# Optimization experiments

Measured on AMD Instinct MI355X. Metric: run time of the kernel, lower is better.

## Reference

```python
import jax, jax.numpy as jnp
import numpy as np

DIM = 768
NUM_HEADS = 12
DIM_HEAD = 64
INNER = NUM_HEADS * DIM_HEAD  # 768
SCALE = DIM_HEAD ** -0.5


def setup_inputs() -> dict:
    key = jax.random.key(0)
    k1, k2, k3 = jax.random.split(key, 3)
    B, N = 8, 1024
    x = jax.random.normal(k1, (B, N, DIM), dtype=jnp.float32)
    # Linear(dim, 3*inner_dim, bias=False): weight shape (out, in) torch-style
    w_qkv = jax.random.normal(k2, (3 * INNER, DIM), dtype=jnp.float32) * (DIM ** -0.5)
    # proj: Linear(inner_dim, dim, bias=False)
    w_proj = jax.random.normal(k3, (DIM, INNER), dtype=jnp.float32) * (INNER ** -0.5)
    return {"x": x, "w_qkv": w_qkv, "w_proj": w_proj}


def reference(x, w_qkv, w_proj):
    B, N, C = x.shape
    H, dh = NUM_HEADS, DIM_HEAD
    # qkv projection: (B,N,C) @ (C, 3*inner) -> (B,N,3*inner)
    qkv = jnp.einsum('bnc,oc->bno', x, w_qkv)
    qkv = qkv.reshape(B, N, 3, H, dh).transpose(2, 0, 3, 1, 4)  # (3,B,H,N,dh)
    q, k, v = qkv[0], qkv[1], qkv[2]
    # attention scores (B,H,N,N)
    attn_scores = jnp.einsum('bhnd,bhmd->bhnm', q, k) * SCALE
    attn_probs = jax.nn.softmax(attn_scores, axis=-1)
    # attention output (B,H,N,dh) -> (B,N,inner)
    attn_out = jnp.einsum('bhnm,bhmd->bhnd', attn_probs, v)
    attn_out = attn_out.transpose(0, 2, 1, 3).reshape(B, N, H * dh)
    out = jnp.einsum('bni,oi->bno', attn_out, w_proj)
    return out
```

## Files before the change

kernel.cpp:

```cpp
#include <hip/hip_runtime.h>
#include <stdint.h>

typedef unsigned short u16;
typedef __attribute__((ext_vector_type(8))) short short8;
typedef __attribute__((ext_vector_type(4))) float f32x4;

#define LOG2E 1.44269504088896340736f

#define Bb 8
#define NSEQ 1024
#define DIMC 768
#define NH 12
#define DH 64
#define INNER 768
#define MTOT (Bb*NSEQ)
#define QKVN (3*INNER)
#define HEADS_TOT (Bb*NH)
#define QKV_PART ((size_t)Bb*NH*NSEQ*DH)

static __device__ inline u16 f2bf(float f) {
    uint32_t u = __builtin_bit_cast(uint32_t, f);
    uint32_t r = (u + 0x7fffu + ((u >> 16) & 1u)) >> 16;
    return (u16)r;
}

typedef __attribute__((address_space(1))) const void gas_void;
typedef __attribute__((address_space(3))) void las_void;
static __device__ __forceinline__ void async16(u16* lds, const u16* g) {
    __builtin_amdgcn_global_load_lds((gas_void*)(uintptr_t)g,
                                     (las_void*)(uintptr_t)lds, 16, 0, 0);
}

#define NX8  786432
#define NWQ8 221184
#define NWP8 73728
#define NCVT (NX8 + NWQ8 + NWP8)
__global__ __launch_bounds__(256) void cvt_all(const float* __restrict__ x,
                                               const float* __restrict__ wq,
                                               const float* __restrict__ wp,
                                               u16* __restrict__ xb,
                                               u16* __restrict__ wqb,
                                               u16* __restrict__ wpb) {
    int i = blockIdx.x * 256 + threadIdx.x;
    const float* s; u16* d; int j;
    if (i < NX8) { s = x; d = xb; j = i; }
    else if (i < NX8 + NWQ8) { s = wq; d = wqb; j = i - NX8; }
    else { s = wp; d = wpb; j = i - NX8 - NWQ8; }
    const float4* s4 = (const float4*)s;
    float4 a = s4[2 * j], b = s4[2 * j + 1];
    float v[8] = {a.x, a.y, a.z, a.w, b.x, b.y, b.z, b.w};
    u16 o[8];
#pragma unroll
    for (int t = 0; t < 8; t++) o[t] = f2bf(v[t]);
    ((uint4*)d)[j] = *(const uint4*)o;
}

#define BM 128
#define BN 128
#define BK 32

template <int MODE>
__global__ __launch_bounds__(256) void gemm_bt(const u16* __restrict__ A,
                                               const u16* __restrict__ Bm,
                                               void* __restrict__ Cout,
                                               int M, int N, int K) {
    __shared__ u16 As[BM * BK];
    __shared__ u16 Bs[BN * BK];
    const int tid = threadIdx.x;
    const int w = tid >> 6, lane = tid & 63, quad = lane >> 4, l16 = lane & 15;
    const int wr = w >> 1, wc = w & 1;
    const int m0 = blockIdx.y * BM;
    const int n0 = blockIdx.x * BN;

    const int rl = lane >> 2, cc = lane & 3;
    const u16* ag[2]; const u16* bg[2]; u16* al[2]; u16* bl[2];
#pragma unroll
    for (int j = 0; j < 2; j++) {
        int r = w * 32 + j * 16 + rl;
        int c = ((cc - ((r >> 1) & 3)) & 3) * 8;
        ag[j] = A + (size_t)(m0 + r) * K + c;
        bg[j] = Bm + (size_t)(n0 + r) * K + c;
        al[j] = As + (w * 32 + j * 16) * BK;
        bl[j] = Bs + (w * 32 + j * 16) * BK;
    }

    const int swz = ((quad + ((l16 >> 1) & 3)) & 3) * 8;
    int aoff[4], boff[4];
#pragma unroll
    for (int t = 0; t < 4; t++) {
        aoff[t] = (wr * 64 + t * 16 + l16) * BK + swz;
        boff[t] = (wc * 64 + t * 16 + l16) * BK + swz;
    }

    f32x4 acc[4][4] = {};
    for (int kt = 0; kt < K; kt += BK) {
        __syncthreads();
#pragma unroll
        for (int j = 0; j < 2; j++) {
            async16(al[j], ag[j] + kt);
            async16(bl[j], bg[j] + kt);
        }
        __syncthreads();
        short8 af[4], bf[4];
#pragma unroll
        for (int t = 0; t < 4; t++) af[t] = *(const short8*)(As + aoff[t]);
#pragma unroll
        for (int t = 0; t < 4; t++) bf[t] = *(const short8*)(Bs + boff[t]);
#pragma unroll
        for (int mt = 0; mt < 4; mt++)
#pragma unroll
            for (int nt = 0; nt < 4; nt++)
                acc[mt][nt] = __builtin_amdgcn_mfma_f32_16x16x32_bf16(af[mt], bf[nt],
                                                                      acc[mt][nt], 0, 0, 0);
    }

    if (MODE == 0) {
        u16* qkv = (u16*)Cout;
#pragma unroll
        for (int nt = 0; nt < 4; nt++) {
            int o = n0 + wc * 64 + nt * 16 + l16;
            int which = o / 768;
            int rem = o - which * 768;
            int h = rem >> 6, d = rem & 63;
            if (which == 2) {
                u16* vt = qkv + 2 * QKV_PART;
#pragma unroll
                for (int mt = 0; mt < 4; mt++) {
                    int m = m0 + wr * 64 + mt * 16 + quad * 4;
                    int bb = m >> 10, ns = m & 1023;
                    alignas(8) u16 pk[4];
#pragma unroll
                    for (int r = 0; r < 4; r++) pk[r] = f2bf(acc[mt][nt][r]);
                    *(uint2*)(vt + ((size_t)(bb * NH + h) * DH + d) * NSEQ + ns) =
                        *(const uint2*)pk;
                }
            } else {
                float sc = (which == 0) ? (0.125f * LOG2E) : 1.0f;
#pragma unroll
                for (int mt = 0; mt < 4; mt++)
#pragma unroll
                    for (int r = 0; r < 4; r++) {
                        int m = m0 + wr * 64 + mt * 16 + quad * 4 + r;
                        int bb = m >> 10, ns = m & 1023;
                        size_t idx = (size_t)which * QKV_PART +
                                     (((size_t)(bb * NH + h) * NSEQ + ns) << 6) + d;
                        qkv[idx] = f2bf(acc[mt][nt][r] * sc);
                    }
            }
        }
    } else {
        float* Co = (float*)Cout;
#pragma unroll
        for (int mt = 0; mt < 4; mt++)
#pragma unroll
            for (int nt = 0; nt < 4; nt++) {
                int o = n0 + wc * 64 + nt * 16 + l16;
#pragma unroll
                for (int r = 0; r < 4; r++) {
                    int m = m0 + wr * 64 + mt * 16 + quad * 4 + r;
                    Co[(size_t)m * N + o] = acc[mt][nt][r];
                }
            }
    }
}

__global__ __launch_bounds__(256) void attn_kernel(const u16* __restrict__ qkv,
                                                   u16* __restrict__ attn) {
    __shared__ u16 Ks[64 * 64];
    __shared__ u16 Vs[64 * 64];
    __shared__ u16 Plds[4][32 * 72];

    const int tid = threadIdx.x;
    const int w = tid >> 6, lane = tid & 63, quad = lane >> 4, l16 = lane & 15;
    const int bh = blockIdx.y;
    const int qt = blockIdx.x;
    const size_t headoff = (size_t)bh * NSEQ * DH;
    const u16* Qp = qkv + headoff;
    const u16* Kp = qkv + QKV_PART + headoff;
    const u16* Vtp = qkv + 2 * QKV_PART + headoff;
    const int q0 = qt * 128 + w * 32;

    const int rl8 = lane >> 3, cc8 = lane & 7;
    const u16* kg[2]; const u16* vg[2]; u16* kl[2]; u16* vl[2];
#pragma unroll
    for (int j = 0; j < 2; j++) {
        int r = w * 16 + j * 8 + rl8;
        int c = ((cc8 - r) & 7) * 8;
        kg[j] = Kp + (size_t)r * DH + c;
        vg[j] = Vtp + (size_t)r * NSEQ + c;
        kl[j] = Ks + (w * 16 + j * 8) * 64;
        vl[j] = Vs + (w * 16 + j * 8) * 64;
    }

    const int sw0 = ((quad + l16) & 7) * 8;
    const int sw1 = ((quad + 4 + l16) & 7) * 8;

    short8 qf[2][2];
#pragma unroll
    for (int mf = 0; mf < 2; mf++) {
        qf[mf][0] = *(const short8*)(Qp + (size_t)(q0 + mf * 16 + l16) * DH + quad * 8);
        qf[mf][1] = *(const short8*)(Qp + (size_t)(q0 + mf * 16 + l16) * DH + 32 + quad * 8);
    }

    f32x4 oacc[2][4] = {};
    float lsum[2][4] = {};

    for (int kt = 0; kt < NSEQ; kt += 64) {
        __syncthreads();
#pragma unroll
        for (int j = 0; j < 2; j++) {
            async16(kl[j], kg[j] + (size_t)kt * DH);
            async16(vl[j], vg[j] + kt);
        }
        __syncthreads();

        u16* Pw0 = Plds[w];
#pragma unroll
        for (int mf = 0; mf < 2; mf++) {
            f32x4 s[4];
#pragma unroll
            for (int nt = 0; nt < 4; nt++) {
                const u16* kr = Ks + (nt * 16 + l16) * 64;
                short8 kf0 = *(const short8*)(kr + sw0);
                short8 kf1 = *(const short8*)(kr + sw1);
                f32x4 z = {};
                z = __builtin_amdgcn_mfma_f32_16x16x32_bf16(qf[mf][0], kf0, z, 0, 0, 0);
                z = __builtin_amdgcn_mfma_f32_16x16x32_bf16(qf[mf][1], kf1, z, 0, 0, 0);
                s[nt] = z;
            }

            u16* Pw = Pw0 + mf * 16 * 72;
#pragma unroll
            for (int nt = 0; nt < 4; nt++)
#pragma unroll
                for (int r = 0; r < 4; r++) {
                    float p = __builtin_amdgcn_exp2f(s[nt][r]);
                    lsum[mf][r] += p;
                    Pw[(quad * 4 + r) * 72 + nt * 16 + l16] = f2bf(p);
                }
            short8 pa0 = *(const short8*)(Pw + l16 * 72 + quad * 8);
            short8 pa1 = *(const short8*)(Pw + l16 * 72 + 32 + quad * 8);

#pragma unroll
            for (int nt = 0; nt < 4; nt++) {
                const u16* vr = Vs + (nt * 16 + l16) * 64;
                short8 vf0 = *(const short8*)(vr + sw0);
                short8 vf1 = *(const short8*)(vr + sw1);
                oacc[mf][nt] = __builtin_amdgcn_mfma_f32_16x16x32_bf16(pa0, vf0,
                                                                       oacc[mf][nt], 0, 0, 0);
                oacc[mf][nt] = __builtin_amdgcn_mfma_f32_16x16x32_bf16(pa1, vf1,
                                                                       oacc[mf][nt], 0, 0, 0);
            }
        }
    }

#pragma unroll
    for (int mf = 0; mf < 2; mf++)
#pragma unroll
        for (int r = 0; r < 4; r++) {
            float v = lsum[mf][r];
#pragma unroll
            for (int mask = 1; mask < 16; mask <<= 1)
                v += __shfl_xor(v, mask, 16);
            lsum[mf][r] = 1.0f / v;
        }

    const int b = bh / NH, h = bh - (bh / NH) * NH;
#pragma unroll
    for (int mf = 0; mf < 2; mf++)
#pragma unroll
        for (int nt = 0; nt < 4; nt++)
#pragma unroll
            for (int r = 0; r < 4; r++) {
                int q = q0 + mf * 16 + quad * 4 + r;
                int d = nt * 16 + l16;
                float val = oacc[mf][nt][r] * lsum[mf][r];
                attn[((size_t)(b * NSEQ + q)) * INNER + h * DH + d] = f2bf(val);
            }
}

extern "C" void kernel_launch(void* const* d_in, const int* in_sizes, int n_in,
                              void* d_out, int out_size, void* d_ws, size_t ws_size,
                              hipStream_t stream) {
    const float* x = (const float*)d_in[0];
    const float* w_qkv = (const float*)d_in[1];
    const float* w_proj = (const float*)d_in[2];
    float* out = (float*)d_out;

    u16* xb = (u16*)d_ws;
    u16* wqkvb = xb + 6291456;
    u16* wprojb = wqkvb + 1769472;
    u16* qkvb = wprojb + 589824;
    u16* attnb = qkvb + 18874368;

    cvt_all<<<NCVT / 256, 256, 0, stream>>>(x, w_qkv, w_proj, xb, wqkvb, wprojb);

    dim3 g1(QKVN / BN, MTOT / BM);
    gemm_bt<0><<<g1, 256, 0, stream>>>(xb, wqkvb, qkvb, MTOT, QKVN, DIMC);

    dim3 g2(NSEQ / 128, HEADS_TOT);
    attn_kernel<<<g2, 256, 0, stream>>>(qkvb, attnb);

    dim3 g3(INNER / BN, MTOT / BM);
    gemm_bt<1><<<g3, 256, 0, stream>>>(attnb, wprojb, out, MTOT, INNER, DIMC);
}
```

Baseline: 205.9 us.

## Keep attention probabilities in registers via transposed S and widen QKV GEMM tile

The attention kernel now computes S transposed (K as the A operand, Q as B), so each lane's exp2 outputs line up with the 16x16x16 bf16 MFMA operand layout. P then feeds the PV product straight from registers, which removes the per-wave LDS round trip for P. K and V fragments are loaded once per key tile and shared across both query sub-tiles. The QKV GEMM moves to a 128x256 tile with 512 threads, and the output conversion uses packed bf16 stores. The costs are higher register pressure and a bf16 rounding change (round-half-up through pkbf), plus a fallback inline-asm MFMA path if the builtin is missing.

```diff
diff --git a/kernel.cpp b/kernel.cpp
--- a/kernel.cpp
+++ b/kernel.cpp
@@ -3,6 +3,7 @@
 
 typedef unsigned short u16;
 typedef __attribute__((ext_vector_type(8))) short short8;
+typedef __attribute__((ext_vector_type(4))) short short4v;
 typedef __attribute__((ext_vector_type(4))) float f32x4;
 
 #define LOG2E 1.44269504088896340736f
@@ -23,6 +24,24 @@
     uint32_t r = (u + 0x7fffu + ((u >> 16) & 1u)) >> 16;
     return (u16)r;
 }
+
+static __device__ __forceinline__ uint32_t pkbf(float f0, float f1) {
+    uint32_t u0 = __builtin_bit_cast(uint32_t, f0) + 0x8000u;
+    uint32_t u1 = __builtin_bit_cast(uint32_t, f1) + 0x8000u;
+    return __builtin_amdgcn_perm(u1, u0, 0x07060302u);
+}
+
+#if __has_builtin(__builtin_amdgcn_mfma_f32_16x16x16bf16_1k)
+static __device__ __forceinline__ f32x4 mfma16(short4v a, short4v b, f32x4 c) {
+    return __builtin_amdgcn_mfma_f32_16x16x16bf16_1k(a, b, c, 0, 0, 0);
+}
+#else
+static __device__ __forceinline__ f32x4 mfma16(short4v a, short4v b, f32x4 c) {
+    asm volatile("v_mfma_f32_16x16x16_bf16 %0, %1, %2, %0\n\ts_nop 7\n\ts_nop 7"
+                 : "+v"(c) : "v"(a), "v"(b));
+    return c;
+}
+#endif
 
 typedef __attribute__((address_space(1))) const void gas_void;
 typedef __attribute__((address_space(3))) void las_void;
@@ -55,22 +74,104 @@
     ((uint4*)d)[j] = *(const uint4*)o;
 }
 
-#define BM 128
-#define BN 128
 #define BK 32
-
-template <int MODE>
-__global__ __launch_bounds__(256) void gemm_bt(const u16* __restrict__ A,
-                                               const u16* __restrict__ Bm,
-                                               void* __restrict__ Cout,
-                                               int M, int N, int K) {
-    __shared__ u16 As[BM * BK];
-    __shared__ u16 Bs[BN * BK];
+__global__ __launch_bounds__(512, 4) void gemm_qkv(const u16* __restrict__ A,
+                                                   const u16* __restrict__ Bm,
+                                                   u16* __restrict__ qkv) {
+    __shared__ u16 As[128 * BK];
+    __shared__ u16 Bs[256 * BK];
+    const int tid = threadIdx.x;
+    const int w = tid >> 6, lane = tid & 63, quad = lane >> 4, l16 = lane & 15;
+    const int wr = w >> 2, wc = w & 3;
+    const int m0 = blockIdx.y * 128;
+    const int n0 = blockIdx.x * 256;
+    const int K = DIMC;
+
+    const int rl = lane >> 2, cc = lane & 3;
+    const int ra = w * 16 + rl;
+    const u16* agp = A + (size_t)(m0 + ra) * K + ((cc - ((ra >> 1) & 3)) & 3) * 8;
+    u16* alp = As + (w * 16) * BK;
+    const u16* bgp[2]; u16* blp[2];
+#pragma unroll
+    for (int j = 0; j < 2; j++) {
+        int rb = w * 32 + j * 16 + rl;
+        bgp[j] = Bm + (size_t)(n0 + rb) * K + ((cc - ((rb >> 1) & 3)) & 3) * 8;
+        blp[j] = Bs + (w * 32 + j * 16) * BK;
+    }
+
+    const int swz = ((quad + ((l16 >> 1) & 3)) & 3) * 8;
+    int aoff[4], boff[4];
+#pragma unroll
+    for (int t = 0; t < 4; t++) {
+        aoff[t] = (wr * 64 + t * 16 + l16) * BK + swz;
+        boff[t] = (wc * 64 + t * 16 + l16) * BK + swz;
+    }
+
+    f32x4 acc[4][4] = {};
+    for (int kt = 0; kt < K; kt += BK) {
+        __syncthreads();
+        async16(alp, agp + kt);
+        async16(blp[0], bgp[0] + kt);
+        async16(blp[1], bgp[1] + kt);
+        __syncthreads();
+        short8 af[4], bf[4];
+#pragma unroll
+        for (int t = 0; t < 4; t++) af[t] = *(const short8*)(As + aoff[t]);
+#pragma unroll
+        for (int t = 0; t < 4; t++) bf[t] = *(const short8*)(Bs + boff[t]);
+#pragma unroll
+        for (int mt = 0; mt < 4; mt++)
+#pragma unroll
+            for (int nt = 0; nt < 4; nt++)
+                acc[mt][nt] = __builtin_amdgcn_mfma_f32_16x16x32_bf16(af[mt], bf[nt],
+                                                                      acc[mt][nt], 0, 0, 0);
+    }
+
+#pragma unroll
+    for (int nt = 0; nt < 4; nt++) {
+        int o = n0 + wc * 64 + nt * 16 + l16;
+        int which = o / 768;
+        int rem = o - which * 768;
+        int h = rem >> 6, d = rem & 63;
+        if (which == 2) {
+            u16* vt = qkv + 2 * QKV_PART;
+#pragma unroll
+            for (int mt = 0; mt < 4; mt++) {
+                int m = m0 + wr * 64 + mt * 16 + quad * 4;
+                int bb = m >> 10, ns = m & 1023;
+                alignas(8) u16 pk[4];
+#pragma unroll
+                for (int r = 0; r < 4; r++) pk[r] = f2bf(acc[mt][nt][r]);
+                *(uint2*)(vt + ((size_t)(bb * NH + h) * DH + d) * NSEQ + ns) =
+                    *(const uint2*)pk;
+            }
+        } else {
+            float sc = (which == 0) ? (0.125f * LOG2E) : 1.0f;
+#pragma unroll
+            for (int mt = 0; mt < 4; mt++)
+#pragma unroll
+                for (int r = 0; r < 4; r++) {
+                    int m = m0 + wr * 64 + mt * 16 + quad * 4 + r;
+                    int bb = m >> 10, ns = m & 1023;
+                    size_t idx = (size_t)which * QKV_PART +
+                                 (((size_t)(bb * NH + h) * NSEQ + ns) << 6) + d;
+                    qkv[idx] = f2bf(acc[mt][nt][r] * sc);
+                }
+        }
+    }
+}
+
+__global__ __launch_bounds__(256) void gemm_proj(const u16* __restrict__ A,
+                                                 const u16* __restrict__ Bm,
+                                                 float* __restrict__ Co) {
+    __shared__ u16 As[128 * BK];
+    __shared__ u16 Bs[128 * BK];
     const int tid = threadIdx.x;
     const int w = tid >> 6, lane = tid & 63, quad = lane >> 4, l16 = lane & 15;
     const int wr = w >> 1, wc = w & 1;
-    const int m0 = blockIdx.y * BM;
-    const int n0 = blockIdx.x * BN;
+    const int m0 = blockIdx.y * 128;
+    const int n0 = blockIdx.x * 128;
+    const int K = INNER, N = DIMC;
 
     const int rl = lane >> 2, cc = lane & 3;
     const u16* ag[2]; const u16* bg[2]; u16* al[2]; u16* bl[2];
@@ -83,7 +184,6 @@
         al[j] = As + (w * 32 + j * 16) * BK;
         bl[j] = Bs + (w * 32 + j * 16) * BK;
     }
-
     const int swz = ((quad + ((l16 >> 1) & 3)) & 3) * 8;
     int aoff[4], boff[4];
 #pragma unroll
@@ -113,67 +213,27 @@
                 acc[mt][nt] = __builtin_amdgcn_mfma_f32_16x16x32_bf16(af[mt], bf[nt],
                                                                       acc[mt][nt], 0, 0, 0);
     }
-
-    if (MODE == 0) {
-        u16* qkv = (u16*)Cout;
+#pragma unroll
+    for (int mt = 0; mt < 4; mt++)
 #pragma unroll
         for (int nt = 0; nt < 4; nt++) {
             int o = n0 + wc * 64 + nt * 16 + l16;
-            int which = o / 768;
-            int rem = o - which * 768;
-            int h = rem >> 6, d = rem & 63;
-            if (which == 2) {
-                u16* vt = qkv + 2 * QKV_PART;
-#pragma unroll
-                for (int mt = 0; mt < 4; mt++) {
-                    int m = m0 + wr * 64 + mt * 16 + quad * 4;
-                    int bb = m >> 10, ns = m & 1023;
-                    alignas(8) u16 pk[4];
-#pragma unroll
-                    for (int r = 0; r < 4; r++) pk[r] = f2bf(acc[mt][nt][r]);
-                    *(uint2*)(vt + ((size_t)(bb * NH + h) * DH + d) * NSEQ + ns) =
-                        *(const uint2*)pk;
-                }
-            } else {
-                float sc = (which == 0) ? (0.125f * LOG2E) : 1.0f;
-#pragma unroll
-                for (int mt = 0; mt < 4; mt++)
-#pragma unroll
-                    for (int r = 0; r < 4; r++) {
-                        int m = m0 + wr * 64 + mt * 16 + quad * 4 + r;
-                        int bb = m >> 10, ns = m & 1023;
-                        size_t idx = (size_t)which * QKV_PART +
-                                     (((size_t)(bb * NH + h) * NSEQ + ns) << 6) + d;
-                        qkv[idx] = f2bf(acc[mt][nt][r] * sc);
-                    }
-            }
-        }
-    } else {
-        float* Co = (float*)Cout;
-#pragma unroll
-        for (int mt = 0; mt < 4; mt++)
-#pragma unroll
-            for (int nt = 0; nt < 4; nt++) {
-                int o = n0 + wc * 64 + nt * 16 + l16;
-#pragma unroll
-                for (int r = 0; r < 4; r++) {
-                    int m = m0 + wr * 64 + mt * 16 + quad * 4 + r;
-                    Co[(size_t)m * N + o] = acc[mt][nt][r];
-                }
-            }
-    }
+#pragma unroll
+            for (int r = 0; r < 4; r++) {
+                int m = m0 + wr * 64 + mt * 16 + quad * 4 + r;
+                Co[(size_t)m * N + o] = acc[mt][nt][r];
+            }
+        }
 }
 
 __global__ __launch_bounds__(256) void attn_kernel(const u16* __restrict__ qkv,
                                                    u16* __restrict__ attn) {
     __shared__ u16 Ks[64 * 64];
     __shared__ u16 Vs[64 * 64];
-    __shared__ u16 Plds[4][32 * 72];
 
     const int tid = threadIdx.x;
     const int w = tid >> 6, lane = tid & 63, quad = lane >> 4, l16 = lane & 15;
-    const int bh = blockIdx.y;
-    const int qt = blockIdx.x;
+    const int bh = blockIdx.y, qt = blockIdx.x;
     const size_t headoff = (size_t)bh * NSEQ * DH;
     const u16* Qp = qkv + headoff;
     const u16* Kp = qkv + QKV_PART + headoff;
@@ -203,7 +263,7 @@
     }
 
     f32x4 oacc[2][4] = {};
-    float lsum[2][4] = {};
+    float lsum[2] = {0.f, 0.f};
 
     for (int kt = 0; kt < NSEQ; kt += 64) {
         __syncthreads();
@@ -214,69 +274,74 @@
         }
         __syncthreads();
 
-        u16* Pw0 = Plds[w];
+        short8 kf[4][2];
+#pragma unroll
+        for (int nt = 0; nt < 4; nt++) {
+            const u16* kr = Ks + (nt * 16 + l16) * 64;
+            kf[nt][0] = *(const short8*)(kr + sw0);
+            kf[nt][1] = *(const short8*)(kr + sw1);
+        }
+        short4v vf[4][4];
+#pragma unroll
+        for (int nt2 = 0; nt2 < 4; nt2++) {
+            int row = nt2 * 16 + l16;
+#pragma unroll
+            for (int c = 0; c < 4; c++) {
+                int off = row * 64 + (((c * 2 + (quad >> 1) + row) & 7) << 3) + (quad & 1) * 4;
+                vf[nt2][c] = *(const short4v*)(Vs + off);
+            }
+        }
+
 #pragma unroll
         for (int mf = 0; mf < 2; mf++) {
-            f32x4 s[4];
+            f32x4 st[4];
 #pragma unroll
             for (int nt = 0; nt < 4; nt++) {
-                const u16* kr = Ks + (nt * 16 + l16) * 64;
-                short8 kf0 = *(const short8*)(kr + sw0);
-                short8 kf1 = *(const short8*)(kr + sw1);
                 f32x4 z = {};
-                z = __builtin_amdgcn_mfma_f32_16x16x32_bf16(qf[mf][0], kf0, z, 0, 0, 0);
-                z = __builtin_amdgcn_mfma_f32_16x16x32_bf16(qf[mf][1], kf1, z, 0, 0, 0);
-                s[nt] = z;
-            }
-
-            u16* Pw = Pw0 + mf * 16 * 72;
-#pragma unroll
-            for (int nt = 0; nt < 4; nt++)
-#pragma unroll
-                for (int r = 0; r < 4; r++) {
-                    float p = __builtin_amdgcn_exp2f(s[nt][r]);
-                    lsum[mf][r] += p;
-                    Pw[(quad * 4 + r) * 72 + nt * 16 + l16] = f2bf(p);
-                }
-            short8 pa0 = *(const short8*)(Pw + l16 * 72 + quad * 8);
-            short8 pa1 = *(const short8*)(Pw + l16 * 72 + 32 + quad * 8);
-
-#pragma unroll
-            for (int nt = 0; nt < 4; nt++) {
-                const u16* vr = Vs + (nt * 16 + l16) * 64;
-                short8 vf0 = *(const short8*)(vr + sw0);
-                short8 vf1 = *(const short8*)(vr + sw1);
-                oacc[mf][nt] = __builtin_amdgcn_mfma_f32_16x16x32_bf16(pa0, vf0,
-                                                                       oacc[mf][nt], 0, 0, 0);
-                oacc[mf][nt] = __builtin_amdgcn_mfma_f32_16x16x32_bf16(pa1, vf1,
-                                                                       oacc[mf][nt], 0, 0, 0);
-            }
-        }
-    }
-
-#pragma unroll
-    for (int mf = 0; mf < 2; mf++)
-#pragma unroll
-        for (int r = 0; r < 4; r++) {
-            float v = lsum[mf][r];
-#pragma unroll
-            for (int mask = 1; mask < 16; mask <<= 1)
-                v += __shfl_xor(v, mask, 16);
-            lsum[mf][r] = 1.0f / v;
-        }
+                z = __builtin_amdgcn_mfma_f32_16x16x32_bf16(kf[nt][0], qf[mf][0], z, 0, 0, 0);
+                z = __builtin_amdgcn_mfma_f32_16x16x32_bf16(kf[nt][1], qf[mf][1], z, 0, 0, 0);
+                st[nt] = z;
+            }
+            short4v pf[4];
+#pragma unroll
+            for (int c = 0; c < 4; c++) {
+                float p0 = __builtin_amdgcn_exp2f(st[c][0]);
+                float p1 = __builtin_amdgcn_exp2f(st[c][1]);
+                float p2 = __builtin_amdgcn_exp2f(st[c][2]);
+                float p3 = __builtin_amdgcn_exp2f(st[c][3]);
+                lsum[mf] += (p0 + p1) + (p2 + p3);
+                uint2 u = {pkbf(p0, p1), pkbf(p2, p3)};
+                pf[c] = __builtin_bit_cast(short4v, u);
+            }
+#pragma unroll
+            for (int nt2 = 0; nt2 < 4; nt2++)
+#pragma unroll
+                for (int c = 0; c < 4; c++)
+                    oacc[mf][nt2] = mfma16(vf[nt2][c], pf[c], oacc[mf][nt2]);
+        }
+    }
+
+#pragma unroll
+    for (int mf = 0; mf < 2; mf++) {
+        float v = lsum[mf];
+        v += __shfl_xor(v, 16);
+        v += __shfl_xor(v, 32);
+        lsum[mf] = 1.0f / v;
+    }
 
     const int b = bh / NH, h = bh - (bh / NH) * NH;
 #pragma unroll
-    for (int mf = 0; mf < 2; mf++)
-#pragma unroll
-        for (int nt = 0; nt < 4; nt++)
-#pragma unroll
-            for (int r = 0; r < 4; r++) {
-                int q = q0 + mf * 16 + quad * 4 + r;
-                int d = nt * 16 + l16;
-                float val = oacc[mf][nt][r] * lsum[mf][r];
-                attn[((size_t)(b * NSEQ + q)) * INNER + h * DH + d] = f2bf(val);
-            }
+    for (int mf = 0; mf < 2; mf++) {
+        int q = q0 + mf * 16 + l16;
+        float inv = lsum[mf];
+#pragma unroll
+        for (int nt2 = 0; nt2 < 4; nt2++) {
+            uint2 u = {pkbf(oacc[mf][nt2][0] * inv, oacc[mf][nt2][1] * inv),
+                       pkbf(oacc[mf][nt2][2] * inv, oacc[mf][nt2][3] * inv)};
+            int d = nt2 * 16 + quad * 4;
+            *(uint2*)(attn + ((size_t)(b * NSEQ + q)) * INNER + h * DH + d) = u;
+        }
+    }
 }
 
 extern "C" void kernel_launch(void* const* d_in, const int* in_sizes, int n_in,
@@ -295,12 +360,12 @@
 
     cvt_all<<<NCVT / 256, 256, 0, stream>>>(x, w_qkv, w_proj, xb, wqkvb, wprojb);
 
-    dim3 g1(QKVN / BN, MTOT / BM);
-    gemm_bt<0><<<g1, 256, 0, stream>>>(xb, wqkvb, qkvb, MTOT, QKVN, DIMC);
+    dim3 g1(QKVN / 256, MTOT / 128);
+    gemm_qkv<<<g1, 512, 0, stream>>>(xb, wqkvb, qkvb);
 
     dim3 g2(NSEQ / 128, HEADS_TOT);
     attn_kernel<<<g2, 256, 0, stream>>>(qkvb, attnb);
 
-    dim3 g3(INNER / BN, MTOT / BM);
-    gemm_bt<1><<<g3, 256, 0, stream>>>(attnb, wprojb, out, MTOT, INNER, DIMC);
-}
+    dim3 g3(INNER / 128, MTOT / 128);
+    gemm_proj<<<g3, 256, 0, stream>>>(attnb, wprojb, out);
+}
```

Measured after the change: 207.1 us. No clear change (+0.6%).
